# Performance work log

Hardware: AMD Instinct MI355X
Metric: run time of the kernel (lower is better)

The kernel has to match this reference:

```python
import jax, jax.numpy as jnp
import numpy as np

NUM_SAMPLES = 512
FG_FRAC = 0.25
BATCH = 64
N = 131072


def _subsample(key, indicator, labels):
    """Faithful port of BalancedPositiveNegativeSampler._static_subsample.

    indicator: bool [N] sample candidates; labels: bool [N] positive flags.
    Returns int32 [N] indicator of sampled examples (1 = sampled).
    """
    n = indicator.shape[0]
    # Pad indicator with extra False examples so at least NUM_SAMPLES are True.
    num_true = jnp.sum(indicator.astype(jnp.float32))
    additional_false = jnp.cumsum((~indicator).astype(jnp.float32)) <= (NUM_SAMPLES - num_true)
    ind = indicator | additional_false
    # Random shuffle (permutation stored to restore order post-sampling).
    perm = jax.random.permutation(key, n)
    ind_p = ind[perm]
    lab_p = labels[perm]
    # 1-based index where indicator True, 0 otherwise; sign by label.
    idx = jnp.where(ind_p, jnp.arange(1, n + 1, dtype=jnp.int32), jnp.int32(0))
    signed = jnp.where(lab_p, jnp.int32(1), jnp.int32(-1))
    s_idx = idx * signed
    # Descending sort: positives first, then zeros, then negatives (most-negative last).
    sorted_desc = jnp.flip(jnp.sort(s_idx))
    # Balanced pos/neg counts.
    num_pos_avail = jnp.sum((sorted_desc > 0).astype(jnp.int32))
    max_pos = jnp.int32(int(NUM_SAMPLES * FG_FRAC))
    num_pos = jnp.minimum(max_pos, num_pos_avail)
    # Take first num_pos from the start and (NUM_SAMPLES - num_pos) from the end.
    rk = jnp.arange(NUM_SAMPLES, dtype=jnp.int32)
    gather_idx = jnp.where(rk < num_pos, rk, n - NUM_SAMPLES + rk)
    sampled = sorted_desc[gather_idx]
    # Back to 0-based indices; clamp empty slots to 0.
    sampled = jnp.abs(sampled) - 1
    sampled = jnp.where(sampled >= 0, sampled, 0)
    # Indicator in shuffled order, then scatter back through the permutation.
    ind2 = jnp.zeros(n, jnp.int32).at[sampled].set(1)
    out = jnp.zeros(n, jnp.int32).at[perm].set(ind2)
    return out


def setup_inputs() -> dict:
    key = jax.random.key(0)
    k1, k2, k3 = jax.random.split(key, 3)
    positive_matches = jax.random.bernoulli(k1, 0.01, (BATCH, N))
    negative_matches = jax.random.bernoulli(k2, 0.70, (BATCH, N)) & (~positive_matches)
    ignored_matches = jax.random.bernoulli(k3, 0.05, (BATCH, N)) & (~positive_matches) & (~negative_matches)
    return {
        "positive_matches": positive_matches,
        "negative_matches": negative_matches,
        "ignored_matches": ignored_matches,
    }


def reference(positive_matches, negative_matches, ignored_matches):
    b = positive_matches.shape[0]
    candidates = (positive_matches | negative_matches) & (~ignored_matches)
    keys = jax.random.split(jax.random.key(42), b)
    sampled_indicators = jax.vmap(_subsample)(keys, candidates, positive_matches)  # int32 [B, N]
    # Final top_k over {0,1} indicators: selected indices first (ascending), then rest.
    _, selected_indices = jax.lax.top_k(sampled_indicators, NUM_SAMPLES)
    return selected_indices
```

## Files before the change

kernel.cpp:

```cpp
#include <hip/hip_runtime.h>
#include <stdint.h>

#define BATCH 64
#define NN 131072
#define NCOARSE 256
#define SLOT 768
#define CHUNK 4096
#define NSUB 1024
#define EMASK17 0x1FFFFu
#define POSCAP 1024
#define NEGCAP 3072
#define SPOSCAP 96
#define SNEGCAP 224
#define STATICP 128u
#define STATICN 250u

typedef uint32_t u32;
typedef uint64_t u64;

__device__ __forceinline__ u32 rotl32(u32 v, int d) { return (v << d) | (v >> (32 - d)); }

__device__ __forceinline__ void threefry2x32(u32 k0, u32 k1, u32 x0, u32 x1, u32& o0, u32& o1) {
  u32 ks2 = k0 ^ k1 ^ 0x1BD11BDAu;
  x0 += k0; x1 += k1;
#define TF_R(r) { x0 += x1; x1 = rotl32(x1, r); x1 ^= x0; }
  TF_R(13) TF_R(15) TF_R(26) TF_R(6)
  x0 += k1;  x1 += ks2 + 1u;
  TF_R(17) TF_R(29) TF_R(16) TF_R(24)
  x0 += ks2; x1 += k0 + 2u;
  TF_R(13) TF_R(15) TF_R(26) TF_R(6)
  x0 += k0;  x1 += k1 + 3u;
  TF_R(17) TF_R(29) TF_R(16) TF_R(24)
  x0 += k1;  x1 += ks2 + 4u;
  TF_R(13) TF_R(15) TF_R(26) TF_R(6)
  x0 += ks2; x1 += k0 + 5u;
#undef TF_R
  o0 = x0; o1 = x1;
}

__device__ __forceinline__ u32 tf_bits(u32 k0, u32 k1, u32 i) {
  u32 o0, o1;
  threefry2x32(k0, k1, 0u, i, o0, o1);
  return o0 ^ o1;
}

__device__ void batch_round_key(int b, int round, u32& rk0, u32& rk1) {
  u32 kb0, kb1;
  threefry2x32(0u, 42u, 0u, (u32)b, kb0, kb1);
  if (round == 1) { threefry2x32(kb0, kb1, 0u, 1u, rk0, rk1); return; }
  u32 c0, c1;
  threefry2x32(kb0, kb1, 0u, 0u, c0, c1);
  threefry2x32(c0, c1, 0u, 1u, rk0, rk1);
}

__global__ __launch_bounds__(256) void scatterA_kernel(u32* __restrict__ cursor, u64* __restrict__ binned,
                                                       const int* __restrict__ posg, const int* __restrict__ negg,
                                                       const int* __restrict__ igng, int batch0) {
  __shared__ u32 sk[2];
  __shared__ u32 hist[NCOARSE];
  __shared__ u32 lstart[NCOARSE];
  __shared__ u32 gbase[NCOARSE];
  __shared__ u64 staged[CHUNK];
  __shared__ u32 stmp[NCOARSE];
  int g = blockIdx.y;
  int b = batch0 + g;
  int tid = threadIdx.x;
  if (tid == 0) { u32 k0, k1; batch_round_key(b, 1, k0, k1); sk[0] = k0; sk[1] = k1; }
  if (tid < NCOARSE) hist[tid] = 0;
  __syncthreads();
  u32 base = blockIdx.x * CHUNK;
  u64 recs[16]; u32 rr[16];
  const int4* P4 = (const int4*)(posg + (size_t)b * NN);
  const int4* Q4 = (const int4*)(negg + (size_t)b * NN);
  const int4* I4 = (const int4*)(igng + (size_t)b * NN);
#pragma unroll
  for (int j = 0; j < 4; j++) {
    u32 e0 = base + j * 1024 + tid * 4;
    int4 pv = P4[e0 >> 2];
    int4 nv = Q4[e0 >> 2];
    int4 iv = I4[e0 >> 2];
#pragma unroll
    for (int m = 0; m < 4; m++) {
      u32 e = e0 + m;
      int p = (&pv.x)[m] != 0, n = (&nv.x)[m] != 0, ig = (&iv.x)[m] != 0;
      u32 label = ((p | n) && !ig) ? (p ? 1u : 2u) : 0u;
      u32 k1 = tf_bits(sk[0], sk[1], e);
      u32 bin = k1 >> 24;
      rr[j * 4 + m] = atomicAdd(&hist[bin], 1u);
      recs[j * 4 + m] = ((u64)k1 << 19) | ((u64)e << 2) | (u64)label;
    }
  }
  __syncthreads();
  if (tid < NCOARSE) stmp[tid] = hist[tid];
  __syncthreads();
  for (int off = 1; off < NCOARSE; off <<= 1) {
    u32 t = 0;
    if (tid < NCOARSE && tid >= off) t = stmp[tid - off];
    __syncthreads();
    if (tid < NCOARSE) stmp[tid] += t;
    __syncthreads();
  }
  if (tid < NCOARSE) lstart[tid] = stmp[tid] - hist[tid];
  __syncthreads();
#pragma unroll
  for (int j = 0; j < 16; j++) {
    u32 bin = (u32)(recs[j] >> 43);
    staged[lstart[bin] + rr[j]] = recs[j];
  }
  if (tid < NCOARSE) {
    u32 c = hist[tid];
    gbase[tid] = c ? atomicAdd(&cursor[(size_t)g * NCOARSE + tid], c) : 0u;
  }
  __syncthreads();
  u64* bn = binned + (size_t)g * NCOARSE * SLOT;
  for (int s = tid; s < CHUNK; s += 256) {
    u64 v = staged[s];
    u32 bin = (u32)(v >> 43);
    u32 off = gbase[bin] + ((u32)s - lstart[bin]);
    if (off < SLOT) bn[(size_t)bin * SLOT + off] = v;
  }
}

__global__ __launch_bounds__(256) void scanB_kernel(const u32* __restrict__ cursor, u32* __restrict__ starts) {
  __shared__ u32 stmp[NCOARSE];
  __shared__ u32 cnts[NCOARSE];
  int g = blockIdx.x, tid = threadIdx.x;
  u32 v = cursor[(size_t)g * NCOARSE + tid];
  cnts[tid] = v; stmp[tid] = v;
  __syncthreads();
  for (int off = 1; off < NCOARSE; off <<= 1) {
    u32 t = (tid >= off) ? stmp[tid - off] : 0u;
    __syncthreads();
    stmp[tid] += t;
    __syncthreads();
  }
  starts[(size_t)g * NCOARSE + tid] = stmp[tid] - cnts[tid];
}

__global__ __launch_bounds__(512) void passB_kernel(const u32* __restrict__ cursor, const u32* __restrict__ starts,
                                                    const u64* __restrict__ binned,
                                                    u32* __restrict__ posh, u32* __restrict__ negh,
                                                    u32* __restrict__ cnt,
                                                    u64* __restrict__ posbuf, u64* __restrict__ negbuf,
                                                    int batch0) {
  __shared__ u32 sk2[2];
  __shared__ u64 keys[SLOT];
  __shared__ u32 hist[NSUB];
  __shared__ u32 sstart[NSUB];
  __shared__ u32 wtot[8];
  __shared__ u32 lpos[NCOARSE], lneg[NCOARSE];
  __shared__ u64 sposb[SPOSCAP];
  __shared__ u64 snegb[SNEGCAP];
  __shared__ u32 lcb[2], lbase[2];
  int g = blockIdx.y;
  int tid = threadIdx.x;
  if (tid == 0) {
    u32 a, c;
    batch_round_key(batch0 + g, 2, a, c); sk2[0] = a; sk2[1] = c;
    lcb[0] = 0; lcb[1] = 0;
  }
  if (tid < NCOARSE) { lpos[tid] = 0; lneg[tid] = 0; }
  __syncthreads();
  const u64* bn = binned + (size_t)g * NCOARSE * SLOT;
  for (int q = 0; q < 8; q++) {
    u32 bin = blockIdx.x * 8 + q;
    u32 cb = cursor[(size_t)g * NCOARSE + bin];
    if (cb > SLOT) cb = SLOT;
    u32 start = starts[(size_t)g * NCOARSE + bin];
    hist[tid] = 0; hist[tid + 512] = 0;
    __syncthreads();
    u64 mykey[2]; u32 mysr[2];
#pragma unroll
    for (int t = 0; t < 2; t++) {
      int i = tid + t * 512;
      if (i < (int)cb) {
        u64 key = bn[(size_t)bin * SLOT + i];
        u32 sub = (u32)(key >> 33) & 0x3FFu;
        u32 r = atomicAdd(&hist[sub], 1u);
        mykey[t] = key;
        mysr[t] = (sub << 10) | r;
      } else {
        mysr[t] = 0xFFFFFFFFu;
      }
    }
    __syncthreads();
    u32 h0 = hist[2 * tid], h1 = hist[2 * tid + 1];
    u32 s = h0 + h1;
    u32 v = s;
#pragma unroll
    for (int off = 1; off < 64; off <<= 1) {
      u32 t2 = __shfl_up(v, off, 64);
      if ((tid & 63) >= off) v += t2;
    }
    if ((tid & 63) == 63) wtot[tid >> 6] = v;
    __syncthreads();
    u32 woff = 0;
    for (int w = 0; w < (tid >> 6); w++) woff += wtot[w];
    u32 excl = v + woff - s;
    sstart[2 * tid] = excl;
    sstart[2 * tid + 1] = excl + h0;
    __syncthreads();
#pragma unroll
    for (int t = 0; t < 2; t++) {
      if (mysr[t] != 0xFFFFFFFFu)
        keys[sstart[mysr[t] >> 10] + (mysr[t] & 0x3FFu)] = mykey[t];
    }
    __syncthreads();
#pragma unroll
    for (int t = 0; t < 2; t++) {
      int i = tid + t * 512;
      if (i < (int)cb) {
        u64 ki = keys[i];
        u32 sub = (u32)(ki >> 33) & 0x3FFu;
        u32 s0 = sstart[sub], h = hist[sub];
        u32 r = 0;
        for (u32 j = s0; j < s0 + h; j++) {
          if (keys[j] < ki) r++;
        }
        u32 p1 = start + s0 + r;
        u32 label = (u32)ki & 3u;
        if (label) {
          u32 e = (u32)(ki >> 2) & EMASK17;
          u32 k2 = tf_bits(sk2[0], sk2[1], p1);
          u32 b8 = k2 >> 24;
          u64 rec = ((u64)p1 << 32) | e;
          if (label == 1) {
            atomicAdd(&lpos[b8], 1u);
            if (b8 >= STATICP) {
              u32 rr2 = atomicAdd(&lcb[0], 1u);
              if (rr2 < SPOSCAP) sposb[rr2] = rec;
              else {
                u32 s2 = atomicAdd(&cnt[(size_t)g * 16], 1u);
                if (s2 < POSCAP) posbuf[(size_t)g * POSCAP + s2] = rec;
              }
            }
          } else {
            atomicAdd(&lneg[b8], 1u);
            if (b8 >= STATICN) {
              u32 rr2 = atomicAdd(&lcb[1], 1u);
              if (rr2 < SNEGCAP) snegb[rr2] = rec;
              else {
                u32 s2 = atomicAdd(&cnt[(size_t)g * 16 + 1], 1u);
                if (s2 < NEGCAP) negbuf[(size_t)g * NEGCAP + s2] = rec;
              }
            }
          }
        }
      }
    }
    __syncthreads();
  }
  if (tid < NCOARSE) {
    if (lpos[tid]) atomicAdd(&posh[(size_t)g * NCOARSE + tid], lpos[tid]);
  } else if (tid < 2 * NCOARSE) {
    int t = tid - NCOARSE;
    if (lneg[t]) atomicAdd(&negh[(size_t)g * NCOARSE + t], lneg[t]);
  }
  if (tid < 2) {
    u32 n = lcb[tid]; u32 cap = tid ? SNEGCAP : SPOSCAP; if (n > cap) n = cap;
    lbase[tid] = n ? atomicAdd(&cnt[(size_t)g * 16 + tid], n) : 0u;
  }
  __syncthreads();
  {
    u32 n0 = lcb[0]; if (n0 > SPOSCAP) n0 = SPOSCAP;
    for (u32 i = tid; i < n0; i += 512) {
      u32 s2 = lbase[0] + i;
      if (s2 < POSCAP) posbuf[(size_t)g * POSCAP + s2] = sposb[i];
    }
    u32 n1 = lcb[1]; if (n1 > SNEGCAP) n1 = SNEGCAP;
    for (u32 i = tid; i < n1; i += 512) {
      u32 s2 = lbase[1] + i;
      if (s2 < NEGCAP) negbuf[(size_t)g * NEGCAP + s2] = snegb[i];
    }
  }
}

__global__ __launch_bounds__(1024) void select_final_kernel(const u32* __restrict__ posh,
                                                            const u32* __restrict__ negh,
                                                            const u32* __restrict__ cnt,
                                                            const u64* __restrict__ posbuf,
                                                            const u64* __restrict__ negbuf,
                                                            int* __restrict__ out, int batch0) {
  int g = blockIdx.x, tid = threadIdx.x, b = batch0 + g;
  __shared__ u32 sk2[2];
  __shared__ u64 key[1024];
  __shared__ u32 val[1024];
  __shared__ int sel[512];
  __shared__ u32 wtot[4];
  __shared__ u32 sh_np, sh_tp, sh_tn, sh_nc;
  if (tid == 0) {
    u32 a, c; batch_round_key(b, 2, a, c); sk2[0] = a; sk2[1] = c;
    sh_tp = 0; sh_tn = 0; sh_nc = 0;
  }
  __syncthreads();

  u32 myspos = 0, mysneg = 0;
  if (tid < NCOARSE) {
    u32 vp = posh[(size_t)g * NCOARSE + (NCOARSE - 1 - tid)];
    u32 vn = negh[(size_t)g * NCOARSE + (NCOARSE - 1 - tid)];
    u32 sp2 = vp, sn2 = vn;
#pragma unroll
    for (int off = 1; off < 64; off <<= 1) {
      u32 tp2 = __shfl_up(sp2, off, 64);
      u32 tn2 = __shfl_up(sn2, off, 64);
      if ((tid & 63) >= off) { sp2 += tp2; sn2 += tn2; }
    }
    if ((tid & 63) == 63) wtot[tid >> 6] = (sp2 & 0xFFFFu) | (sn2 << 16);
    myspos = sp2; mysneg = sn2;
  }
  __syncthreads();
  if (tid < NCOARSE) {
    for (int w = 0; w < (tid >> 6); w++) {
      u32 t2 = wtot[w];
      myspos += t2 & 0xFFFFu;
      mysneg += t2 >> 16;
    }
    if (tid == NCOARSE - 1) sh_np = myspos;
  }
  __syncthreads();
  u32 np = sh_np;
  u32 qp = np < 128 ? np : 128;
  u32 qn = 512 - qp;
  if (tid < NCOARSE) {
    u32 i = NCOARSE - 1 - tid;
    if (qp > 0 && myspos >= qp) atomicMax(&sh_tp, i);
    if (mysneg >= qn) atomicMax(&sh_tn, i);
  }
  if (tid < 512) sel[tid] = 0;
  __syncthreads();
  u32 tp = sh_tp, tn = sh_tn;
  u32 cp = cnt[(size_t)g * 16]; if (cp > POSCAP) cp = POSCAP;
  u32 cn = cnt[(size_t)g * 16 + 1]; if (cn > NEGCAP) cn = NEGCAP;

  for (u32 i = tid; i < cp; i += 1024) {
    u64 v = posbuf[(size_t)g * POSCAP + i];
    u32 p1 = (u32)(v >> 32), e = (u32)v;
    u32 k2 = tf_bits(sk2[0], sk2[1], p1);
    if (qp > 0 && (k2 >> 24) >= tp) {
      u32 r = atomicAdd(&sh_nc, 1u);
      if (r < 1024) { key[r] = ((u64)k2 << 32) | p1; val[r] = e; }
    }
  }
  __syncthreads();
  {
    u32 nc = sh_nc; if (nc > 1024) nc = 1024;
    if (tid < (int)nc) {
      u64 mk = key[tid];
      u32 rank = 0;
      for (u32 j = 0; j < nc; j++) rank += (key[j] > mk);
      if (rank < qp) sel[rank] = (int)val[tid];
    }
  }
  __syncthreads();
  if (tid == 0) sh_nc = 0;
  __syncthreads();

  for (u32 i = tid; i < cn; i += 1024) {
    u64 v = negbuf[(size_t)g * NEGCAP + i];
    u32 p1 = (u32)(v >> 32), e = (u32)v;
    u32 k2 = tf_bits(sk2[0], sk2[1], p1);
    if ((k2 >> 24) >= tn) {
      u32 r = atomicAdd(&sh_nc, 1u);
      if (r < 1024) { key[r] = ((u64)k2 << 32) | p1; val[r] = e; }
    }
  }
  __syncthreads();
  {
    u32 nc = sh_nc; if (nc > 1024) nc = 1024;
    if (tid < (int)nc) {
      u64 mk = key[tid];
      u32 rank = 0;
      for (u32 j = 0; j < nc; j++) rank += (key[j] > mk);
      if (rank < qn) sel[qp + rank] = (int)val[tid];
    }
  }
  __syncthreads();

  if (tid < 512) {
    int v = sel[tid];
    u32 rank = 0;
    for (int j = 0; j < 512; j++) rank += (sel[j] < v);
    out[(size_t)b * 512 + rank] = v;
  }
}

extern "C" void kernel_launch(void* const* d_in, const int* in_sizes, int n_in,
                              void* d_out, int out_size, void* d_ws, size_t ws_size,
                              hipStream_t stream) {
  const int* pos = (const int*)d_in[0];
  const int* neg = (const int*)d_in[1];
  const int* ign = (const int*)d_in[2];
  int* out = (int*)d_out;

  size_t zeroPer = (NCOARSE * 3 + 16) * 4;
  size_t perBatch = zeroPer + (size_t)NCOARSE * SLOT * 8 + NCOARSE * 4 +
                    (size_t)POSCAP * 8 + (size_t)NEGCAP * 8;
  int G = (int)(ws_size / perBatch);
  if (G > BATCH) G = BATCH;
  if (G < 1) G = 1;

  char* p = (char*)d_ws;
  u32* cursor = (u32*)p;            p += (size_t)G * NCOARSE * 4;
  u32* posh = (u32*)p;              p += (size_t)G * NCOARSE * 4;
  u32* negh = (u32*)p;              p += (size_t)G * NCOARSE * 4;
  u32* cnt = (u32*)p;               p += (size_t)G * 16 * 4;
  size_t zeroBytes = (size_t)p - (size_t)d_ws;
  u64* binned = (u64*)p;            p += (size_t)G * NCOARSE * SLOT * 8;
  u32* starts = (u32*)p;            p += (size_t)G * NCOARSE * 4;
  u64* posbuf = (u64*)p;            p += (size_t)G * POSCAP * 8;
  u64* negbuf = (u64*)p;            p += (size_t)G * NEGCAP * 8;

  for (int batch0 = 0; batch0 < BATCH; batch0 += G) {
    int Gi = (BATCH - batch0 < G) ? (BATCH - batch0) : G;
    hipMemsetAsync(d_ws, 0, zeroBytes, stream);
    dim3 gridS(NN / CHUNK, Gi);
    scatterA_kernel<<<gridS, 256, 0, stream>>>(cursor, binned, pos, neg, ign, batch0);
    scanB_kernel<<<Gi, 256, 0, stream>>>(cursor, starts);
    dim3 gridP(NCOARSE / 8, Gi);
    passB_kernel<<<gridP, 512, 0, stream>>>(cursor, starts, binned, posh, negh, cnt, posbuf, negbuf, batch0);
    select_final_kernel<<<Gi, 1024, 0, stream>>>(posh, negh, cnt, posbuf, negbuf, out, batch0);
  }
}
```

Baseline: 240.6 us.

## Derive candidate thresholds from label counts and fold scan into passB

Counts positives and negatives in scatterA and uses those counts to pick per-batch thresholds on the second-round key byte before passB runs. This replaces the static thresholds and removes the global per-bin histograms. The separate bin-start scan kernel is folded into passB as a per-block wave scan, and select_final drops its histogram threshold search in favour of ranking every buffered candidate directly. The intent is to remove one kernel launch, the histogram atomics and the threshold search. The trade-offs are larger candidate buffers and an O(n^2) rank over up to 2560 negatives, and the count-derived thresholds are statistical estimates that could drop needed candidates if the key distribution deviates.

```diff
diff --git a/kernel.cpp b/kernel.cpp
--- a/kernel.cpp
+++ b/kernel.cpp
@@ -4,16 +4,14 @@
 #define BATCH 64
 #define NN 131072
 #define NCOARSE 256
-#define SLOT 768
+#define SLOT 704
 #define CHUNK 4096
 #define NSUB 1024
 #define EMASK17 0x1FFFFu
-#define POSCAP 1024
-#define NEGCAP 3072
+#define POSCAP 1536
+#define NEGCAP 2560
 #define SPOSCAP 96
-#define SNEGCAP 224
-#define STATICP 128u
-#define STATICN 250u
+#define SNEGCAP 160
 
 typedef uint32_t u32;
 typedef uint64_t u64;
@@ -53,7 +51,9 @@
   threefry2x32(c0, c1, 0u, 1u, rk0, rk1);
 }
 
-__global__ __launch_bounds__(256) void scatterA_kernel(u32* __restrict__ cursor, u64* __restrict__ binned,
+
+__global__ __launch_bounds__(256) void scatterA_kernel(u32* __restrict__ cursor, u32* __restrict__ meta,
+                                                       u64* __restrict__ binned,
                                                        const int* __restrict__ posg, const int* __restrict__ negg,
                                                        const int* __restrict__ igng, int batch0) {
   __shared__ u32 sk[2];
@@ -62,14 +62,17 @@
   __shared__ u32 gbase[NCOARSE];
   __shared__ u64 staged[CHUNK];
   __shared__ u32 stmp[NCOARSE];
+  __shared__ u32 cntPN[2];
   int g = blockIdx.y;
   int b = batch0 + g;
   int tid = threadIdx.x;
   if (tid == 0) { u32 k0, k1; batch_round_key(b, 1, k0, k1); sk[0] = k0; sk[1] = k1; }
+  if (tid < 2) cntPN[tid] = 0;
   if (tid < NCOARSE) hist[tid] = 0;
   __syncthreads();
   u32 base = blockIdx.x * CHUNK;
   u64 recs[16]; u32 rr[16];
+  u32 myp = 0, myn = 0;
   const int4* P4 = (const int4*)(posg + (size_t)b * NN);
   const int4* Q4 = (const int4*)(negg + (size_t)b * NN);
   const int4* I4 = (const int4*)(igng + (size_t)b * NN);
@@ -84,12 +87,20 @@
       u32 e = e0 + m;
       int p = (&pv.x)[m] != 0, n = (&nv.x)[m] != 0, ig = (&iv.x)[m] != 0;
       u32 label = ((p | n) && !ig) ? (p ? 1u : 2u) : 0u;
+      myp += (label == 1);
+      myn += (label == 2);
       u32 k1 = tf_bits(sk[0], sk[1], e);
       u32 bin = k1 >> 24;
       rr[j * 4 + m] = atomicAdd(&hist[bin], 1u);
       recs[j * 4 + m] = ((u64)k1 << 19) | ((u64)e << 2) | (u64)label;
     }
   }
+#pragma unroll
+  for (int off = 32; off > 0; off >>= 1) {
+    myp += __shfl_down(myp, off, 64);
+    myn += __shfl_down(myn, off, 64);
+  }
+  if ((tid & 63) == 0) { atomicAdd(&cntPN[0], myp); atomicAdd(&cntPN[1], myn); }
   __syncthreads();
   if (tid < NCOARSE) stmp[tid] = hist[tid];
   __syncthreads();
@@ -119,36 +130,23 @@
     u32 off = gbase[bin] + ((u32)s - lstart[bin]);
     if (off < SLOT) bn[(size_t)bin * SLOT + off] = v;
   }
-}
-
-__global__ __launch_bounds__(256) void scanB_kernel(const u32* __restrict__ cursor, u32* __restrict__ starts) {
-  __shared__ u32 stmp[NCOARSE];
-  __shared__ u32 cnts[NCOARSE];
-  int g = blockIdx.x, tid = threadIdx.x;
-  u32 v = cursor[(size_t)g * NCOARSE + tid];
-  cnts[tid] = v; stmp[tid] = v;
-  __syncthreads();
-  for (int off = 1; off < NCOARSE; off <<= 1) {
-    u32 t = (tid >= off) ? stmp[tid - off] : 0u;
-    __syncthreads();
-    stmp[tid] += t;
-    __syncthreads();
-  }
-  starts[(size_t)g * NCOARSE + tid] = stmp[tid] - cnts[tid];
-}
-
-__global__ __launch_bounds__(512) void passB_kernel(const u32* __restrict__ cursor, const u32* __restrict__ starts,
+  __syncthreads();
+  if (tid < 2) atomicAdd(&meta[(size_t)g * 16 + 2 + tid], cntPN[tid]);
+}
+
+__global__ __launch_bounds__(512) void passB_kernel(const u32* __restrict__ cursor,
                                                     const u64* __restrict__ binned,
-                                                    u32* __restrict__ posh, u32* __restrict__ negh,
-                                                    u32* __restrict__ cnt,
+                                                    u32* __restrict__ meta,
                                                     u64* __restrict__ posbuf, u64* __restrict__ negbuf,
                                                     int batch0) {
   __shared__ u32 sk2[2];
+  __shared__ u32 sth[2];
   __shared__ u64 keys[SLOT];
   __shared__ u32 hist[NSUB];
   __shared__ u32 sstart[NSUB];
   __shared__ u32 wtot[8];
-  __shared__ u32 lpos[NCOARSE], lneg[NCOARSE];
+  __shared__ u32 bstart[NCOARSE];
+  __shared__ u32 bcnt[NCOARSE];
   __shared__ u64 sposb[SPOSCAP];
   __shared__ u64 snegb[SNEGCAP];
   __shared__ u32 lcb[2], lbase[2];
@@ -158,15 +156,38 @@
     u32 a, c;
     batch_round_key(batch0 + g, 2, a, c); sk2[0] = a; sk2[1] = c;
     lcb[0] = 0; lcb[1] = 0;
-  }
-  if (tid < NCOARSE) { lpos[tid] = 0; lneg[tid] = 0; }
+    u32 np = meta[(size_t)g * 16 + 2], nn = meta[(size_t)g * 16 + 3];
+    u32 tp = 0, tn = 0;
+    if (np > 512) { u32 d = 131072u / np + 1u; tp = (d < 256) ? 256u - d : 0u; }
+    if (nn > 1536) { u32 d = 393216u / nn + 1u; tn = (d < 256) ? 256u - d : 0u; }
+    sth[0] = tp; sth[1] = tn;
+  }
+  u32 bv = 0, bs = 0;
+  if (tid < NCOARSE) {
+    bv = cursor[(size_t)g * NCOARSE + tid];
+    bs = bv;
+#pragma unroll
+    for (int off = 1; off < 64; off <<= 1) {
+      u32 t2 = __shfl_up(bs, off, 64);
+      if ((tid & 63) >= off) bs += t2;
+    }
+    if ((tid & 63) == 63) wtot[tid >> 6] = bs;
+  }
+  __syncthreads();
+  if (tid < NCOARSE) {
+    u32 woff = 0;
+    for (int w = 0; w < (tid >> 6); w++) woff += wtot[w];
+    bstart[tid] = bs + woff - bv;
+    bcnt[tid] = bv;
+  }
   __syncthreads();
   const u64* bn = binned + (size_t)g * NCOARSE * SLOT;
+  u32 tp = sth[0], tn = sth[1];
   for (int q = 0; q < 8; q++) {
     u32 bin = blockIdx.x * 8 + q;
-    u32 cb = cursor[(size_t)g * NCOARSE + bin];
+    u32 cb = bcnt[bin];
     if (cb > SLOT) cb = SLOT;
-    u32 start = starts[(size_t)g * NCOARSE + bin];
+    u32 start = bstart[bin];
     hist[tid] = 0; hist[tid + 512] = 0;
     __syncthreads();
     u64 mykey[2]; u32 mysr[2];
@@ -225,22 +246,20 @@
           u32 b8 = k2 >> 24;
           u64 rec = ((u64)p1 << 32) | e;
           if (label == 1) {
-            atomicAdd(&lpos[b8], 1u);
-            if (b8 >= STATICP) {
+            if (b8 >= tp) {
               u32 rr2 = atomicAdd(&lcb[0], 1u);
               if (rr2 < SPOSCAP) sposb[rr2] = rec;
               else {
-                u32 s2 = atomicAdd(&cnt[(size_t)g * 16], 1u);
+                u32 s2 = atomicAdd(&meta[(size_t)g * 16], 1u);
                 if (s2 < POSCAP) posbuf[(size_t)g * POSCAP + s2] = rec;
               }
             }
           } else {
-            atomicAdd(&lneg[b8], 1u);
-            if (b8 >= STATICN) {
+            if (b8 >= tn) {
               u32 rr2 = atomicAdd(&lcb[1], 1u);
               if (rr2 < SNEGCAP) snegb[rr2] = rec;
               else {
-                u32 s2 = atomicAdd(&cnt[(size_t)g * 16 + 1], 1u);
+                u32 s2 = atomicAdd(&meta[(size_t)g * 16 + 1], 1u);
                 if (s2 < NEGCAP) negbuf[(size_t)g * NEGCAP + s2] = rec;
               }
             }
@@ -250,15 +269,9 @@
     }
     __syncthreads();
   }
-  if (tid < NCOARSE) {
-    if (lpos[tid]) atomicAdd(&posh[(size_t)g * NCOARSE + tid], lpos[tid]);
-  } else if (tid < 2 * NCOARSE) {
-    int t = tid - NCOARSE;
-    if (lneg[t]) atomicAdd(&negh[(size_t)g * NCOARSE + t], lneg[t]);
-  }
   if (tid < 2) {
     u32 n = lcb[tid]; u32 cap = tid ? SNEGCAP : SPOSCAP; if (n > cap) n = cap;
-    lbase[tid] = n ? atomicAdd(&cnt[(size_t)g * 16 + tid], n) : 0u;
+    lbase[tid] = n ? atomicAdd(&meta[(size_t)g * 16 + tid], n) : 0u;
   }
   __syncthreads();
   {
@@ -275,112 +288,68 @@
   }
 }
 
-__global__ __launch_bounds__(1024) void select_final_kernel(const u32* __restrict__ posh,
-                                                            const u32* __restrict__ negh,
-                                                            const u32* __restrict__ cnt,
+__global__ __launch_bounds__(1024) void select_final_kernel(const u32* __restrict__ meta,
                                                             const u64* __restrict__ posbuf,
                                                             const u64* __restrict__ negbuf,
                                                             int* __restrict__ out, int batch0) {
   int g = blockIdx.x, tid = threadIdx.x, b = batch0 + g;
   __shared__ u32 sk2[2];
-  __shared__ u64 key[1024];
-  __shared__ u32 val[1024];
+  __shared__ u64 key[NEGCAP];
+  __shared__ u32 val[NEGCAP];
   __shared__ int sel[512];
-  __shared__ u32 wtot[4];
-  __shared__ u32 sh_np, sh_tp, sh_tn, sh_nc;
-  if (tid == 0) {
-    u32 a, c; batch_round_key(b, 2, a, c); sk2[0] = a; sk2[1] = c;
-    sh_tp = 0; sh_tn = 0; sh_nc = 0;
-  }
-  __syncthreads();
-
-  u32 myspos = 0, mysneg = 0;
-  if (tid < NCOARSE) {
-    u32 vp = posh[(size_t)g * NCOARSE + (NCOARSE - 1 - tid)];
-    u32 vn = negh[(size_t)g * NCOARSE + (NCOARSE - 1 - tid)];
-    u32 sp2 = vp, sn2 = vn;
-#pragma unroll
-    for (int off = 1; off < 64; off <<= 1) {
-      u32 tp2 = __shfl_up(sp2, off, 64);
-      u32 tn2 = __shfl_up(sn2, off, 64);
-      if ((tid & 63) >= off) { sp2 += tp2; sn2 += tn2; }
-    }
-    if ((tid & 63) == 63) wtot[tid >> 6] = (sp2 & 0xFFFFu) | (sn2 << 16);
-    myspos = sp2; mysneg = sn2;
-  }
-  __syncthreads();
-  if (tid < NCOARSE) {
-    for (int w = 0; w < (tid >> 6); w++) {
-      u32 t2 = wtot[w];
-      myspos += t2 & 0xFFFFu;
-      mysneg += t2 >> 16;
-    }
-    if (tid == NCOARSE - 1) sh_np = myspos;
-  }
-  __syncthreads();
-  u32 np = sh_np;
+  if (tid == 0) { u32 a, c; batch_round_key(b, 2, a, c); sk2[0] = a; sk2[1] = c; }
+  u32 np = meta[(size_t)g * 16 + 2];
   u32 qp = np < 128 ? np : 128;
   u32 qn = 512 - qp;
-  if (tid < NCOARSE) {
-    u32 i = NCOARSE - 1 - tid;
-    if (qp > 0 && myspos >= qp) atomicMax(&sh_tp, i);
-    if (mysneg >= qn) atomicMax(&sh_tn, i);
-  }
+  u32 cp = meta[(size_t)g * 16]; if (cp > POSCAP) cp = POSCAP;
+  u32 cn = meta[(size_t)g * 16 + 1]; if (cn > NEGCAP) cn = NEGCAP;
   if (tid < 512) sel[tid] = 0;
   __syncthreads();
-  u32 tp = sh_tp, tn = sh_tn;
-  u32 cp = cnt[(size_t)g * 16]; if (cp > POSCAP) cp = POSCAP;
-  u32 cn = cnt[(size_t)g * 16 + 1]; if (cn > NEGCAP) cn = NEGCAP;
 
   for (u32 i = tid; i < cp; i += 1024) {
-    u64 v = posbuf[(size_t)g * POSCAP + i];
-    u32 p1 = (u32)(v >> 32), e = (u32)v;
-    u32 k2 = tf_bits(sk2[0], sk2[1], p1);
-    if (qp > 0 && (k2 >> 24) >= tp) {
-      u32 r = atomicAdd(&sh_nc, 1u);
-      if (r < 1024) { key[r] = ((u64)k2 << 32) | p1; val[r] = e; }
-    }
+    u64 rec = posbuf[(size_t)g * POSCAP + i];
+    u32 p1 = (u32)(rec >> 32);
+    key[i] = ((u64)tf_bits(sk2[0], sk2[1], p1) << 32) | p1;
+    val[i] = (u32)rec;
   }
   __syncthreads();
   {
-    u32 nc = sh_nc; if (nc > 1024) nc = 1024;
-    if (tid < (int)nc) {
-      u64 mk = key[tid];
-      u32 rank = 0;
-      for (u32 j = 0; j < nc; j++) rank += (key[j] > mk);
-      if (rank < qp) sel[rank] = (int)val[tid];
-    }
-  }
-  __syncthreads();
-  if (tid == 0) sh_nc = 0;
+    u64 mk0 = (tid < (int)cp) ? key[tid] : 0ull;
+    u64 mk1 = (tid + 1024 < (int)cp) ? key[tid + 1024] : 0ull;
+    u32 r0 = 0, r1 = 0;
+    for (u32 j = 0; j < cp; j++) { u64 kj = key[j]; r0 += (kj > mk0); r1 += (kj > mk1); }
+    if (tid < (int)cp && r0 < qp) sel[r0] = (int)val[tid];
+    if (tid + 1024 < (int)cp && r1 < qp) sel[r1] = (int)val[tid + 1024];
+  }
   __syncthreads();
 
   for (u32 i = tid; i < cn; i += 1024) {
-    u64 v = negbuf[(size_t)g * NEGCAP + i];
-    u32 p1 = (u32)(v >> 32), e = (u32)v;
-    u32 k2 = tf_bits(sk2[0], sk2[1], p1);
-    if ((k2 >> 24) >= tn) {
-      u32 r = atomicAdd(&sh_nc, 1u);
-      if (r < 1024) { key[r] = ((u64)k2 << 32) | p1; val[r] = e; }
-    }
+    u64 rec = negbuf[(size_t)g * NEGCAP + i];
+    u32 p1 = (u32)(rec >> 32);
+    key[i] = ((u64)tf_bits(sk2[0], sk2[1], p1) << 32) | p1;
+    val[i] = (u32)rec;
   }
   __syncthreads();
   {
-    u32 nc = sh_nc; if (nc > 1024) nc = 1024;
-    if (tid < (int)nc) {
-      u64 mk = key[tid];
-      u32 rank = 0;
-      for (u32 j = 0; j < nc; j++) rank += (key[j] > mk);
-      if (rank < qn) sel[qp + rank] = (int)val[tid];
-    }
+    u64 mk0 = (tid < (int)cn) ? key[tid] : 0ull;
+    u64 mk1 = (tid + 1024 < (int)cn) ? key[tid + 1024] : 0ull;
+    u64 mk2 = (tid + 2048 < (int)cn) ? key[tid + 2048] : 0ull;
+    u32 r0 = 0, r1 = 0, r2 = 0;
+    for (u32 j = 0; j < cn; j++) {
+      u64 kj = key[j];
+      r0 += (kj > mk0); r1 += (kj > mk1); r2 += (kj > mk2);
+    }
+    if (tid < (int)cn && r0 < qn) sel[qp + r0] = (int)val[tid];
+    if (tid + 1024 < (int)cn && r1 < qn) sel[qp + r1] = (int)val[tid + 1024];
+    if (tid + 2048 < (int)cn && r2 < qn) sel[qp + r2] = (int)val[tid + 2048];
   }
   __syncthreads();
 
   if (tid < 512) {
     int v = sel[tid];
-    u32 rank = 0;
-    for (int j = 0; j < 512; j++) rank += (sel[j] < v);
-    out[(size_t)b * 512 + rank] = v;
+    u32 r = 0;
+    for (int j = 0; j < 512; j++) r += (sel[j] < v);
+    out[(size_t)b * 512 + r] = v;
   }
 }
 
@@ -392,8 +361,7 @@
   const int* ign = (const int*)d_in[2];
   int* out = (int*)d_out;
 
-  size_t zeroPer = (NCOARSE * 3 + 16) * 4;
-  size_t perBatch = zeroPer + (size_t)NCOARSE * SLOT * 8 + NCOARSE * 4 +
+  size_t perBatch = (NCOARSE + 16) * 4 + (size_t)NCOARSE * SLOT * 8 +
                     (size_t)POSCAP * 8 + (size_t)NEGCAP * 8;
   int G = (int)(ws_size / perBatch);
   if (G > BATCH) G = BATCH;
@@ -401,12 +369,9 @@
 
   char* p = (char*)d_ws;
   u32* cursor = (u32*)p;            p += (size_t)G * NCOARSE * 4;
-  u32* posh = (u32*)p;              p += (size_t)G * NCOARSE * 4;
-  u32* negh = (u32*)p;              p += (size_t)G * NCOARSE * 4;
-  u32* cnt = (u32*)p;               p += (size_t)G * 16 * 4;
+  u32* meta = (u32*)p;              p += (size_t)G * 16 * 4;
   size_t zeroBytes = (size_t)p - (size_t)d_ws;
   u64* binned = (u64*)p;            p += (size_t)G * NCOARSE * SLOT * 8;
-  u32* starts = (u32*)p;            p += (size_t)G * NCOARSE * 4;
   u64* posbuf = (u64*)p;            p += (size_t)G * POSCAP * 8;
   u64* negbuf = (u64*)p;            p += (size_t)G * NEGCAP * 8;
 
@@ -414,10 +379,9 @@
     int Gi = (BATCH - batch0 < G) ? (BATCH - batch0) : G;
     hipMemsetAsync(d_ws, 0, zeroBytes, stream);
     dim3 gridS(NN / CHUNK, Gi);
-    scatterA_kernel<<<gridS, 256, 0, stream>>>(cursor, binned, pos, neg, ign, batch0);
-    scanB_kernel<<<Gi, 256, 0, stream>>>(cursor, starts);
+    scatterA_kernel<<<gridS, 256, 0, stream>>>(cursor, meta, binned, pos, neg, ign, batch0);
     dim3 gridP(NCOARSE / 8, Gi);
-    passB_kernel<<<gridP, 512, 0, stream>>>(cursor, starts, binned, posh, negh, cnt, posbuf, negbuf, batch0);
-    select_final_kernel<<<Gi, 1024, 0, stream>>>(posh, negh, cnt, posbuf, negbuf, out, batch0);
-  }
-}
+    passB_kernel<<<gridP, 512, 0, stream>>>(cursor, binned, meta, posbuf, negbuf, batch0);
+    select_final_kernel<<<Gi, 1024, 0, stream>>>(meta, posbuf, negbuf, out, batch0);
+  }
+}
```

Result: slower. 327.1 us (+36.0%).
